# Kernel optimization log

Hardware: AMD Instinct MI355X
Metric: run time of the kernel (lower is better)

The kernel has to match this reference:

```python
import jax, jax.numpy as jnp
import numpy as np

HIDDEN = 1024
N_HEADS = 16
HEAD_DIM = HIDDEN // N_HEADS  # 64


def setup_inputs() -> dict:
    key = jax.random.key(0)
    k1, k2, k3 = jax.random.split(key, 3)
    x = jax.random.normal(k1, (2, 2048, HIDDEN), dtype=jnp.float32)
    # nn.Linear(hidden, 3*hidden, bias=False): weight [3*hidden, hidden]
    w_qkv = jax.random.normal(k2, (3 * HIDDEN, HIDDEN), dtype=jnp.float32) * (HIDDEN ** -0.5)
    # nn.Linear(hidden, hidden, bias=False): weight [hidden, hidden]
    w_dense = jax.random.normal(k3, (HIDDEN, HIDDEN), dtype=jnp.float32) * (HIDDEN ** -0.5)
    return {"x": x, "w_qkv": w_qkv, "w_dense": w_dense}


def reference(x, w_qkv, w_dense):
    B, S, D = x.shape
    # Fused QKV projection: y = x @ w_qkv.T -> [B, S, 3*D]
    qkv = jnp.einsum("bsd,ed->bse", x, w_qkv)
    q, k, v = jnp.split(qkv, 3, axis=-1)

    def heads(t):  # [B,S,D] -> [B,H,S,hd]
        return t.reshape(B, S, N_HEADS, HEAD_DIM).transpose(0, 2, 1, 3)

    q, k, v = heads(q), heads(k), heads(v)
    scale = jnp.asarray(HEAD_DIM, x.dtype) ** -0.5
    scores = jnp.einsum("bhqd,bhkd->bhqk", q, k) * scale  # [B,H,S,S]
    probs = jax.nn.softmax(scores, axis=-1)
    ctx = jnp.einsum("bhqk,bhkd->bhqd", probs, v)  # [B,H,S,hd]
    ctx = ctx.transpose(0, 2, 1, 3).reshape(B, S, D)
    # Output dense: ctx @ w_dense.T
    return jnp.einsum("bsd,ed->bse", ctx, w_dense)
```

## Files before the change

### kernel.cpp

```cpp
#include <hip/hip_runtime.h>

typedef unsigned short u16;
typedef unsigned int u32;
typedef __bf16 bf16x8 __attribute__((ext_vector_type(8)));
typedef float f32x4 __attribute__((ext_vector_type(4)));
typedef u16 u16x8 __attribute__((ext_vector_type(8)));
typedef u16 u16x4 __attribute__((ext_vector_type(4)));
typedef u32 u32x2 __attribute__((ext_vector_type(2)));

__device__ __forceinline__ u16 to_bf16(float f) {
  unsigned int u = __builtin_bit_cast(unsigned int, f);
  u += 0x7fffu + ((u >> 16) & 1u);
  return (u16)(u >> 16);
}

__device__ __forceinline__ f32x4 mfma16(bf16x8 a, bf16x8 b, f32x4 c) {
  return __builtin_amdgcn_mfma_f32_16x16x32_bf16(a, b, c, 0, 0, 0);
}

#define GLD16(gp, lp) __builtin_amdgcn_global_load_lds( \
    (const __attribute__((address_space(1))) unsigned int*)(gp), \
    (__attribute__((address_space(3))) unsigned int*)(lp), 16, 0, 0)

#define WAITVM(N) asm volatile("s_waitcnt vmcnt(" #N ")" ::: "memory")
#define BARRIER() asm volatile("s_barrier" ::: "memory")
#define MEMFENCE() asm volatile("" ::: "memory")

__global__ __launch_bounds__(256) void cvt_all(
    const float* __restrict__ x, const float* __restrict__ wq, const float* __restrict__ wd,
    u16* __restrict__ xb, u16* __restrict__ wqb, u16* __restrict__ wdb) {
  long i = ((long)blockIdx.x * 256 + threadIdx.x) * 4;
  const float* s; u16* d;
  if (i < 4194304)      { s = x  + i;             d = xb  + i; }
  else if (i < 7340032) { s = wq + (i - 4194304); d = wqb + (i - 4194304); }
  else                  { s = wd + (i - 7340032); d = wdb + (i - 7340032); }
  f32x4 f = *(const f32x4*)s;
  u16x4 o;
  o[0] = to_bf16(f[0]); o[1] = to_bf16(f[1]); o[2] = to_bf16(f[2]); o[3] = to_bf16(f[3]);
  *(u16x4*)d = o;
}

__global__ __launch_bounds__(256) void gemm_qkv(const u16* __restrict__ A,
    const u16* __restrict__ Bt, u16* __restrict__ qk, u16* __restrict__ vt,
    int K, float qscale) {
  __shared__ __align__(16) u16 As[2][4096];
  __shared__ __align__(16) u16 Bs[2][4096];
  const int tid = threadIdx.x;
  const int lane = tid & 63, wave = tid >> 6;
  const int wm = (wave & 1) * 64, wn = (wave >> 1) * 64;
  const int bm = blockIdx.y * 128, bn = blockIdx.x * 128;
  const int fm = lane & 15, fk8 = (lane >> 4) * 8;
  f32x4 acc[4][4] = {};

  const int r0 = tid >> 2, c0 = (tid & 3) * 8;
  const u16* Ag = A + (long)(bm + r0) * K + c0;
  const u16* Bg = Bt + (long)(bn + r0) * K + c0;
  const long rowStep = (long)64 * K;

#define GSTAGE(K0, IB) do { \
    GLD16(Ag + (K0),           &As[IB][tid * 8]); \
    GLD16(Ag + rowStep + (K0), &As[IB][tid * 8 + 2048]); \
    GLD16(Bg + (K0),           &Bs[IB][tid * 8]); \
    GLD16(Bg + rowStep + (K0), &Bs[IB][tid * 8 + 2048]); \
  } while (0)

  GSTAGE(0, 0);
  int ib = 0;
  for (int k0 = 0; k0 < K; k0 += 32) {
    if (k0 + 32 < K) { GSTAGE(k0 + 32, ib ^ 1); WAITVM(4); }
    else             { WAITVM(0); }
    BARRIER();
    bf16x8 a[4], b[4];
#pragma unroll
    for (int i = 0; i < 4; i++) a[i] = *(const bf16x8*)&As[ib][(wm + i * 16 + fm) * 32 + fk8];
#pragma unroll
    for (int j = 0; j < 4; j++) b[j] = *(const bf16x8*)&Bs[ib][(wn + j * 16 + fm) * 32 + fk8];
#pragma unroll
    for (int i = 0; i < 4; i++)
#pragma unroll
      for (int j = 0; j < 4; j++)
        acc[i][j] = mfma16(a[i], b[j], acc[i][j]);
    BARRIER();
    ib ^= 1;
  }
#undef GSTAGE

  const int er = (lane >> 4) * 4, ec = lane & 15;
  if (bn >= 2048) {
#pragma unroll
    for (int i = 0; i < 4; i++) {
      const long row0 = bm + wm + i * 16 + er;
      const long bb = row0 >> 11;
      const int kv = (int)(row0 & 2047);
#pragma unroll
      for (int j = 0; j < 4; j++) {
        const int dcol = bn + wn + j * 16 + ec - 2048;
        u16x4 pk;
#pragma unroll
        for (int r = 0; r < 4; r++) pk[r] = to_bf16(acc[i][j][r]);
        *(u16x4*)&vt[((bb * 16 + (dcol >> 6)) * 64 + (dcol & 63)) * 2048 + kv] = pk;
      }
    }
  } else {
    const float sc = (bn < 1024) ? qscale : 1.0f;
#pragma unroll
    for (int i = 0; i < 4; i++)
#pragma unroll
      for (int j = 0; j < 4; j++)
#pragma unroll
        for (int r = 0; r < 4; r++) {
          long row = bm + wm + i * 16 + er + r;
          long col = bn + wn + j * 16 + ec;
          qk[row * 2048 + col] = to_bf16(acc[i][j][r] * sc);
        }
  }
}

__global__ __launch_bounds__(256) void gemm_bt_n64(const u16* __restrict__ A,
    const u16* __restrict__ Bt, float* __restrict__ C, int M, int N, int K) {
  __shared__ __align__(16) u16 As[2][4096];
  __shared__ __align__(16) u16 Bs[2][2048];
  const int tid = threadIdx.x;
  const int lane = tid & 63, wave = tid >> 6;
  const int wm = (wave & 1) * 64, wn = (wave >> 1) * 32;
  const int bm = blockIdx.y * 128, bn = blockIdx.x * 64;
  const int fm = lane & 15, fk8 = (lane >> 4) * 8;
  f32x4 acc[4][2] = {};

  const int r0 = tid >> 2, c0 = (tid & 3) * 8;
  const u16* Ag = A + (long)(bm + r0) * K + c0;
  const u16* Bg = Bt + (long)(bn + r0) * K + c0;
  const long rowStep = (long)64 * K;

#define GSTAGE(K0, IB) do { \
    GLD16(Ag + (K0),           &As[IB][tid * 8]); \
    GLD16(Ag + rowStep + (K0), &As[IB][tid * 8 + 2048]); \
    GLD16(Bg + (K0),           &Bs[IB][tid * 8]); \
  } while (0)

  GSTAGE(0, 0);
  int ib = 0;
  for (int k0 = 0; k0 < K; k0 += 32) {
    if (k0 + 32 < K) { GSTAGE(k0 + 32, ib ^ 1); WAITVM(3); }
    else             { WAITVM(0); }
    BARRIER();
    bf16x8 a[4], b[2];
#pragma unroll
    for (int i = 0; i < 4; i++) a[i] = *(const bf16x8*)&As[ib][(wm + i * 16 + fm) * 32 + fk8];
#pragma unroll
    for (int j = 0; j < 2; j++) b[j] = *(const bf16x8*)&Bs[ib][(wn + j * 16 + fm) * 32 + fk8];
#pragma unroll
    for (int i = 0; i < 4; i++)
#pragma unroll
      for (int j = 0; j < 2; j++)
        acc[i][j] = mfma16(a[i], b[j], acc[i][j]);
    BARRIER();
    ib ^= 1;
  }
#undef GSTAGE

  const int er = (lane >> 4) * 4, ec = lane & 15;
#pragma unroll
  for (int i = 0; i < 4; i++)
#pragma unroll
    for (int j = 0; j < 2; j++)
#pragma unroll
      for (int r = 0; r < 4; r++)
        C[(long)(bm + wm + i * 16 + er + r) * N + bn + wn + j * 16 + ec] = acc[i][j][r];
}

__global__ __launch_bounds__(256, 2) void attn_kernel(const u16* __restrict__ qk,
                                                      const u16* __restrict__ vt,
                                                      u16* __restrict__ ctx) {
  __shared__ __align__(16) u16 Kb[2][4096];
  __shared__ __align__(16) u16 Vb[2][4096];
  __shared__ __align__(16) u16 Ps[128 * 64];
  const int tid = threadIdx.x, lane = tid & 63, wave = tid >> 6;
  const int fm = lane & 15, g = lane >> 4, f7 = fm & 7;

  const int id = blockIdx.x;
  const int c = id & 7, m = id >> 3;
  const int qt = m & 15, bh = (m >> 4) * 8 + c;
  const int b = bh >> 4, h = bh & 15;
  const long tokBase = (long)b * 2048;
  const int q0 = qt * 128;

  const int sr8 = lane >> 3;
  const int gch = (lane & 7) ^ sr8;
  const u16* Kg = qk + (tokBase + wave * 16 + sr8) * 2048 + 1024 + h * 64 + gch * 8;
  const u16* Vg = vt + ((long)bh * 64 + wave * 16 + sr8) * 2048 + gch * 8;
  u16* KL = &Kb[0][wave * 16 * 64] + lane * 8;
  u16* VL = &Vb[0][wave * 16 * 64] + lane * 8;

#define STAGE(S0, IB) do { \
    GLD16(Kg + (long)(S0) * 2048,          KL + (IB) * 4096); \
    GLD16(Kg + (long)((S0) + 8) * 2048,    KL + (IB) * 4096 + 512); \
    GLD16(Vg + (S0),                       VL + (IB) * 4096); \
    GLD16(Vg + (S0) + (long)8 * 2048,      VL + (IB) * 4096 + 512); \
  } while (0)

  STAGE(0, 0);

  bf16x8 qa[2][2];
#pragma unroll
  for (int t = 0; t < 2; t++) {
    const long qoff = (tokBase + q0 + wave * 32 + t * 16 + fm) * 2048 + h * 64;
    qa[t][0] = *(const bf16x8*)&qk[qoff + g * 8];
    qa[t][1] = *(const bf16x8*)&qk[qoff + 32 + g * 8];
  }

  f32x4 o[2][4] = {};
  f32x4 ol[2] = {};
  u16x8 onesu = {0x3F80, 0x3F80, 0x3F80, 0x3F80, 0x3F80, 0x3F80, 0x3F80, 0x3F80};
  bf16x8 ones = __builtin_bit_cast(bf16x8, onesu);

  int ib = 0;
  for (int s0 = 0; s0 < 2048; s0 += 64) {
    if (s0 + 64 < 2048) { STAGE(s0 + 64, ib ^ 1); WAITVM(4); }
    else                { WAITVM(0); }
    BARRIER();

    const u16* Kt = &Kb[ib][0];
    const u16* Vtile = &Vb[ib][0];

#pragma unroll
    for (int jj = 0; jj < 4; jj++) {
      bf16x8 k0 = *(const bf16x8*)&Kt[(jj * 16 + fm) * 64 + ((g    ) ^ f7) * 8];
      bf16x8 k1 = *(const bf16x8*)&Kt[(jj * 16 + fm) * 64 + ((4 + g) ^ f7) * 8];
#pragma unroll
      for (int t = 0; t < 2; t++) {
        f32x4 s = {};
        s = mfma16(k0, qa[t][0], s);
        s = mfma16(k1, qa[t][1], s);
        u32 p0r = __builtin_bit_cast(u32, __builtin_amdgcn_exp2f(s[0])) + 0x8000u;
        u32 p1r = __builtin_bit_cast(u32, __builtin_amdgcn_exp2f(s[1])) + 0x8000u;
        u32 p2r = __builtin_bit_cast(u32, __builtin_amdgcn_exp2f(s[2])) + 0x8000u;
        u32 p3r = __builtin_bit_cast(u32, __builtin_amdgcn_exp2f(s[3])) + 0x8000u;
        u32x2 wv;
        wv[0] = __builtin_amdgcn_perm(p1r, p0r, 0x07060302u);
        wv[1] = __builtin_amdgcn_perm(p3r, p2r, 0x07060302u);
        const int slot = (jj * 4 + g) ^ (2 * f7);
        *(u32x2*)((u32*)&Ps[(wave * 32 + t * 16 + fm) * 64] + slot * 2) = wv;
      }
    }

    MEMFENCE();

    __builtin_amdgcn_s_setprio(1);
#pragma unroll
    for (int ks = 0; ks < 2; ks++) {
      bf16x8 vb[4];
#pragma unroll
      for (int jd = 0; jd < 4; jd++)
        vb[jd] = *(const bf16x8*)&Vtile[(jd * 16 + fm) * 64 + ((ks * 4 + g) ^ f7) * 8];
#pragma unroll
      for (int t = 0; t < 2; t++) {
        bf16x8 pa = *(const bf16x8*)&Ps[(wave * 32 + t * 16 + fm) * 64 +
                                        ((4 * ks + g) ^ f7) * 8];
#pragma unroll
        for (int jd = 0; jd < 4; jd++)
          o[t][jd] = mfma16(pa, vb[jd], o[t][jd]);
        ol[t] = mfma16(pa, ones, ol[t]);
      }
    }
    __builtin_amdgcn_s_setprio(0);
    BARRIER();
    ib ^= 1;
  }
#undef STAGE

#pragma unroll
  for (int t = 0; t < 2; t++) {
#pragma unroll
    for (int r = 0; r < 4; r++) {
      float inv = 1.0f / ol[t][r];
      const long obase = (tokBase + q0 + wave * 32 + t * 16 + g * 4 + r) * 1024 + h * 64;
#pragma unroll
      for (int jd = 0; jd < 4; jd++)
        ctx[obase + jd * 16 + fm] = to_bf16(o[t][jd][r] * inv);
    }
  }
}

extern "C" void kernel_launch(void* const* d_in, const int* in_sizes, int n_in,
                              void* d_out, int out_size, void* d_ws, size_t ws_size,
                              hipStream_t stream) {
  const float* x  = (const float*)d_in[0];
  const float* wq = (const float*)d_in[1];
  const float* wd = (const float*)d_in[2];
  float* out = (float*)d_out;
  char* ws = (char*)d_ws;
  u16* xb   = (u16*)(ws);
  u16* wqb  = (u16*)(ws + 8388608);
  u16* wdb  = (u16*)(ws + 14680064);
  u16* qkb  = (u16*)(ws + 16777216);
  u16* vtb  = (u16*)(ws + 33554432);
  u16* ctxb = (u16*)(ws + 41943040);

  const float sscale = 0.125f * 1.44269504f;

  cvt_all<<<8192, 256, 0, stream>>>(x, wq, wd, xb, wqb, wdb);
  gemm_qkv<<<dim3(24, 32), 256, 0, stream>>>(xb, wqb, qkb, vtb, 1024, sscale);
  attn_kernel<<<512, 256, 0, stream>>>(qkb, vtb, ctxb);
  gemm_bt_n64<<<dim3(16, 32), 256, 0, stream>>>(ctxb, wdb, out, 4096, 1024, 1024);
}
```

Measured before the change: 179.3 us.

## Keep softmax probabilities in registers and feed PV via 16x16x16 MFMA

```diff
diff --git a/kernel.cpp b/kernel.cpp
--- a/kernel.cpp
+++ b/kernel.cpp
@@ -6,6 +6,7 @@
 typedef float f32x4 __attribute__((ext_vector_type(4)));
 typedef u16 u16x8 __attribute__((ext_vector_type(8)));
 typedef u16 u16x4 __attribute__((ext_vector_type(4)));
+typedef short s16x4 __attribute__((ext_vector_type(4)));
 typedef u32 u32x2 __attribute__((ext_vector_type(2)));
 
 __device__ __forceinline__ u16 to_bf16(float f) {
@@ -18,13 +19,20 @@
   return __builtin_amdgcn_mfma_f32_16x16x32_bf16(a, b, c, 0, 0, 0);
 }
 
+__device__ __forceinline__ f32x4 mfma1k(s16x4 a, s16x4 b, f32x4 c) {
+  return __builtin_amdgcn_mfma_f32_16x16x16bf16_1k(a, b, c, 0, 0, 0);
+}
+
+__device__ __forceinline__ u32 cvtpk(float a, float b) {
+  u32 r; asm("v_cvt_pk_bf16_f32 %0, %1, %2" : "=v"(r) : "v"(a), "v"(b)); return r;
+}
+
 #define GLD16(gp, lp) __builtin_amdgcn_global_load_lds( \
     (const __attribute__((address_space(1))) unsigned int*)(gp), \
     (__attribute__((address_space(3))) unsigned int*)(lp), 16, 0, 0)
 
 #define WAITVM(N) asm volatile("s_waitcnt vmcnt(" #N ")" ::: "memory")
 #define BARRIER() asm volatile("s_barrier" ::: "memory")
-#define MEMFENCE() asm volatile("" ::: "memory")
 
 __global__ __launch_bounds__(256) void cvt_all(
     const float* __restrict__ x, const float* __restrict__ wq, const float* __restrict__ wd,
@@ -174,7 +182,6 @@
                                                       u16* __restrict__ ctx) {
   __shared__ __align__(16) u16 Kb[2][4096];
   __shared__ __align__(16) u16 Vb[2][4096];
-  __shared__ __align__(16) u16 Ps[128 * 64];
   const int tid = threadIdx.x, lane = tid & 63, wave = tid >> 6;
   const int fm = lane & 15, g = lane >> 4, f7 = fm & 7;
 
@@ -211,8 +218,7 @@
 
   f32x4 o[2][4] = {};
   f32x4 ol[2] = {};
-  u16x8 onesu = {0x3F80, 0x3F80, 0x3F80, 0x3F80, 0x3F80, 0x3F80, 0x3F80, 0x3F80};
-  bf16x8 ones = __builtin_bit_cast(bf16x8, onesu);
+  const s16x4 onesb = {0x3F80, 0x3F80, 0x3F80, 0x3F80};
 
   int ib = 0;
   for (int s0 = 0; s0 < 2048; s0 += 64) {
@@ -227,43 +233,33 @@
     for (int jj = 0; jj < 4; jj++) {
       bf16x8 k0 = *(const bf16x8*)&Kt[(jj * 16 + fm) * 64 + ((g    ) ^ f7) * 8];
       bf16x8 k1 = *(const bf16x8*)&Kt[(jj * 16 + fm) * 64 + ((4 + g) ^ f7) * 8];
+      s16x4 pa[2];
 #pragma unroll
       for (int t = 0; t < 2; t++) {
         f32x4 s = {};
         s = mfma16(k0, qa[t][0], s);
         s = mfma16(k1, qa[t][1], s);
-        u32 p0r = __builtin_bit_cast(u32, __builtin_amdgcn_exp2f(s[0])) + 0x8000u;
-        u32 p1r = __builtin_bit_cast(u32, __builtin_amdgcn_exp2f(s[1])) + 0x8000u;
-        u32 p2r = __builtin_bit_cast(u32, __builtin_amdgcn_exp2f(s[2])) + 0x8000u;
-        u32 p3r = __builtin_bit_cast(u32, __builtin_amdgcn_exp2f(s[3])) + 0x8000u;
-        u32x2 wv;
-        wv[0] = __builtin_amdgcn_perm(p1r, p0r, 0x07060302u);
-        wv[1] = __builtin_amdgcn_perm(p3r, p2r, 0x07060302u);
-        const int slot = (jj * 4 + g) ^ (2 * f7);
-        *(u32x2*)((u32*)&Ps[(wave * 32 + t * 16 + fm) * 64] + slot * 2) = wv;
+        u32x2 pk;
+        pk[0] = cvtpk(__builtin_amdgcn_exp2f(s[0]), __builtin_amdgcn_exp2f(s[1]));
+        pk[1] = cvtpk(__builtin_amdgcn_exp2f(s[2]), __builtin_amdgcn_exp2f(s[3]));
+        pa[t] = __builtin_bit_cast(s16x4, pk);
       }
+      s16x4 vb[4];
+#pragma unroll
+      for (int jd = 0; jd < 4; jd++)
+        vb[jd] = __builtin_bit_cast(s16x4, *(const u16x4*)&Vtile[
+            (jd * 16 + fm) * 64 + ((2 * jj + (g >> 1)) ^ f7) * 8 + (g & 1) * 4]);
+
+      __builtin_amdgcn_s_setprio(1);
+#pragma unroll
+      for (int t = 0; t < 2; t++) {
+#pragma unroll
+        for (int jd = 0; jd < 4; jd++)
+          o[t][jd] = mfma1k(pa[t], vb[jd], o[t][jd]);
+        ol[t] = mfma1k(pa[t], onesb, ol[t]);
+      }
+      __builtin_amdgcn_s_setprio(0);
     }
-
-    MEMFENCE();
-
-    __builtin_amdgcn_s_setprio(1);
-#pragma unroll
-    for (int ks = 0; ks < 2; ks++) {
-      bf16x8 vb[4];
-#pragma unroll
-      for (int jd = 0; jd < 4; jd++)
-        vb[jd] = *(const bf16x8*)&Vtile[(jd * 16 + fm) * 64 + ((ks * 4 + g) ^ f7) * 8];
-#pragma unroll
-      for (int t = 0; t < 2; t++) {
-        bf16x8 pa = *(const bf16x8*)&Ps[(wave * 32 + t * 16 + fm) * 64 +
-                                        ((4 * ks + g) ^ f7) * 8];
-#pragma unroll
-        for (int jd = 0; jd < 4; jd++)
-          o[t][jd] = mfma16(pa, vb[jd], o[t][jd]);
-        ol[t] = mfma16(pa, ones, ol[t]);
-      }
-    }
-    __builtin_amdgcn_s_setprio(0);
     BARRIER();
     ib ^= 1;
   }
```

New measurement: 180.1 us. No clear change (+0.5%).

## Keep softmax probabilities in registers instead of staging through LDS

Applied to the files above, without the earlier changes.

```diff
diff --git a/kernel.cpp b/kernel.cpp
--- a/kernel.cpp
+++ b/kernel.cpp
@@ -7,6 +7,7 @@
 typedef u16 u16x8 __attribute__((ext_vector_type(8)));
 typedef u16 u16x4 __attribute__((ext_vector_type(4)));
 typedef u32 u32x2 __attribute__((ext_vector_type(2)));
+typedef u32 u32x4 __attribute__((ext_vector_type(4)));
 
 __device__ __forceinline__ u16 to_bf16(float f) {
   unsigned int u = __builtin_bit_cast(unsigned int, f);
@@ -18,13 +19,16 @@
   return __builtin_amdgcn_mfma_f32_16x16x32_bf16(a, b, c, 0, 0, 0);
 }
 
+__device__ __forceinline__ u32 cvtpk(float a, float b) {
+  u32 r; asm("v_cvt_pk_bf16_f32 %0, %1, %2" : "=v"(r) : "v"(a), "v"(b)); return r;
+}
+
 #define GLD16(gp, lp) __builtin_amdgcn_global_load_lds( \
     (const __attribute__((address_space(1))) unsigned int*)(gp), \
     (__attribute__((address_space(3))) unsigned int*)(lp), 16, 0, 0)
 
 #define WAITVM(N) asm volatile("s_waitcnt vmcnt(" #N ")" ::: "memory")
 #define BARRIER() asm volatile("s_barrier" ::: "memory")
-#define MEMFENCE() asm volatile("" ::: "memory")
 
 __global__ __launch_bounds__(256) void cvt_all(
     const float* __restrict__ x, const float* __restrict__ wq, const float* __restrict__ wd,
@@ -174,7 +178,6 @@
                                                       u16* __restrict__ ctx) {
   __shared__ __align__(16) u16 Kb[2][4096];
   __shared__ __align__(16) u16 Vb[2][4096];
-  __shared__ __align__(16) u16 Ps[128 * 64];
   const int tid = threadIdx.x, lane = tid & 63, wave = tid >> 6;
   const int fm = lane & 15, g = lane >> 4, f7 = fm & 7;
 
@@ -224,46 +227,43 @@
     const u16* Vtile = &Vb[ib][0];
 
 #pragma unroll
-    for (int jj = 0; jj < 4; jj++) {
-      bf16x8 k0 = *(const bf16x8*)&Kt[(jj * 16 + fm) * 64 + ((g    ) ^ f7) * 8];
-      bf16x8 k1 = *(const bf16x8*)&Kt[(jj * 16 + fm) * 64 + ((4 + g) ^ f7) * 8];
+    for (int p = 0; p < 2; p++) {
+      u32x4 pk[2];
+#pragma unroll
+      for (int jh = 0; jh < 2; jh++) {
+        const int jj = 2 * p + jh;
+        bf16x8 k0 = *(const bf16x8*)&Kt[(jj * 16 + fm) * 64 + ((g    ) ^ f7) * 8];
+        bf16x8 k1 = *(const bf16x8*)&Kt[(jj * 16 + fm) * 64 + ((4 + g) ^ f7) * 8];
+#pragma unroll
+        for (int t = 0; t < 2; t++) {
+          f32x4 s = {};
+          s = mfma16(k0, qa[t][0], s);
+          s = mfma16(k1, qa[t][1], s);
+          pk[t][2 * jh + 0] = cvtpk(__builtin_amdgcn_exp2f(s[0]), __builtin_amdgcn_exp2f(s[1]));
+          pk[t][2 * jh + 1] = cvtpk(__builtin_amdgcn_exp2f(s[2]), __builtin_amdgcn_exp2f(s[3]));
+        }
+      }
+      bf16x8 vb[4];
+#pragma unroll
+      for (int jd = 0; jd < 4; jd++) {
+        const int rowb = (jd * 16 + fm) * 64;
+        u32x2 lo = *(const u32x2*)&Vtile[rowb + ((2 * (2 * p)     + (g >> 1)) ^ f7) * 8 + (g & 1) * 4];
+        u32x2 hi = *(const u32x2*)&Vtile[rowb + ((2 * (2 * p + 1) + (g >> 1)) ^ f7) * 8 + (g & 1) * 4];
+        u32x4 v4; v4[0] = lo[0]; v4[1] = lo[1]; v4[2] = hi[0]; v4[3] = hi[1];
+        vb[jd] = __builtin_bit_cast(bf16x8, v4);
+      }
+
+      __builtin_amdgcn_s_setprio(1);
 #pragma unroll
       for (int t = 0; t < 2; t++) {
-        f32x4 s = {};
-        s = mfma16(k0, qa[t][0], s);
-        s = mfma16(k1, qa[t][1], s);
-        u32 p0r = __builtin_bit_cast(u32, __builtin_amdgcn_exp2f(s[0])) + 0x8000u;
-        u32 p1r = __builtin_bit_cast(u32, __builtin_amdgcn_exp2f(s[1])) + 0x8000u;
-        u32 p2r = __builtin_bit_cast(u32, __builtin_amdgcn_exp2f(s[2])) + 0x8000u;
-        u32 p3r = __builtin_bit_cast(u32, __builtin_amdgcn_exp2f(s[3])) + 0x8000u;
-        u32x2 wv;
-        wv[0] = __builtin_amdgcn_perm(p1r, p0r, 0x07060302u);
-        wv[1] = __builtin_amdgcn_perm(p3r, p2r, 0x07060302u);
-        const int slot = (jj * 4 + g) ^ (2 * f7);
-        *(u32x2*)((u32*)&Ps[(wave * 32 + t * 16 + fm) * 64] + slot * 2) = wv;
-      }
-    }
-
-    MEMFENCE();
-
-    __builtin_amdgcn_s_setprio(1);
-#pragma unroll
-    for (int ks = 0; ks < 2; ks++) {
-      bf16x8 vb[4];
-#pragma unroll
-      for (int jd = 0; jd < 4; jd++)
-        vb[jd] = *(const bf16x8*)&Vtile[(jd * 16 + fm) * 64 + ((ks * 4 + g) ^ f7) * 8];
-#pragma unroll
-      for (int t = 0; t < 2; t++) {
-        bf16x8 pa = *(const bf16x8*)&Ps[(wave * 32 + t * 16 + fm) * 64 +
-                                        ((4 * ks + g) ^ f7) * 8];
+        bf16x8 pa = __builtin_bit_cast(bf16x8, pk[t]);
 #pragma unroll
         for (int jd = 0; jd < 4; jd++)
           o[t][jd] = mfma16(pa, vb[jd], o[t][jd]);
         ol[t] = mfma16(pa, ones, ol[t]);
       }
+      __builtin_amdgcn_s_setprio(0);
     }
-    __builtin_amdgcn_s_setprio(0);
     BARRIER();
     ib ^= 1;
   }
```

New measurement: 177.6 us. About the same (-1.0%).
